# Kernel tuning notes

Hardware: AMD Instinct MI355X
Metric: run time of the kernel (lower is better)

## Reference

```python
import jax, jax.numpy as jnp
import numpy as np

N, E, F = 50000, 800000, 256
EPS = 1e-5


def _agg(h, src, dst, n):
    # gather src node features and sum into dst nodes (DGL copy_src + sum reduce)
    return jax.ops.segment_sum(h[src], dst, num_segments=n)


def _gcn_layer(h, src, dst, W, b):
    n = h.shape[0]
    h = _agg(h, src, dst, n)
    h = _agg(h, src, dst, n)  # update_all is called twice per layer
    return h @ W.T + b


def _batchnorm(h, gamma, beta):
    mean = jnp.mean(h, axis=0)
    var = jnp.mean(jnp.square(h - mean), axis=0)  # biased var, training mode
    return (h - mean) * jax.lax.rsqrt(var + EPS) * gamma + beta


def _branch(feature, src, dst, W1, b1, W2, b2, W3, b3, gamma, beta):
    h = _gcn_layer(feature, src, dst, W1, b1)
    h = _batchnorm(h, gamma, beta)
    h = _gcn_layer(h, src, dst, W2, b2)
    h = _gcn_layer(h, src, dst, W3, b3)
    return h


def setup_inputs() -> dict:
    key = jax.random.key(0)
    ks = jax.random.split(key, 12)
    s = 1.0 / np.sqrt(F)
    return {
        "feature": jax.random.normal(ks[0], (N, F), dtype=jnp.float32),
        "src1": jax.random.randint(ks[1], (E,), 0, N, dtype=jnp.int32),
        "dst1": jax.random.randint(ks[2], (E,), 0, N, dtype=jnp.int32),
        "src2": jax.random.randint(ks[3], (E,), 0, N, dtype=jnp.int32),
        "dst2": jax.random.randint(ks[4], (E,), 0, N, dtype=jnp.int32),
        "W1": jax.random.uniform(ks[5], (F, F), jnp.float32, -s, s),
        "b1": jax.random.uniform(ks[6], (F,), jnp.float32, -s, s),
        "W2": jax.random.uniform(ks[7], (F, F), jnp.float32, -s, s),
        "b2": jax.random.uniform(ks[8], (F,), jnp.float32, -s, s),
        "W3": jax.random.uniform(ks[9], (F, F), jnp.float32, -s, s),
        "b3": jax.random.uniform(ks[10], (F,), jnp.float32, -s, s),
        "gamma": jnp.ones((F,), jnp.float32),
        "beta": jnp.zeros((F,), jnp.float32),
    }


def reference(feature, src1, dst1, src2, dst2, W1, b1, W2, b2, W3, b3, gamma, beta):
    h1 = _branch(feature, src1, dst1, W1, b1, W2, b2, W3, b3, gamma, beta)
    h2 = _branch(feature, src2, dst2, W1, b1, W2, b2, W3, b3, gamma, beta)
    return h1.T @ h2  # [F, F]
```

## Files before the change

kernel.cpp:

```cpp
#include <hip/hip_runtime.h>
#include <hip/hip_fp16.h>

#define FDIM 256
#define GRAM_KS 96
#define NB 64


typedef _Float16 f16x8 __attribute__((ext_vector_type(8)));
typedef float f32x4 __attribute__((ext_vector_type(4)));

union H8 { uint2 u2[2]; f16x8 v; };

__device__ __forceinline__ f16x8 ldfrag(const __half* ldsT, int m, int g) {
  H8 h;
  h.u2[0] = *(const uint2*)(ldsT + m * 36 + g * 4);
  h.u2[1] = *(const uint2*)(ldsT + m * 36 + 16 + g * 4);
  return h.v;
}

__device__ __forceinline__ void h8acc(uint4 u, float* a) {
  float2 t;
  t = __half22float2(*(__half2*)&u.x); a[0] += t.x; a[1] += t.y;
  t = __half22float2(*(__half2*)&u.y); a[2] += t.x; a[3] += t.y;
  t = __half22float2(*(__half2*)&u.z); a[4] += t.x; a[5] += t.y;
  t = __half22float2(*(__half2*)&u.w); a[6] += t.x; a[7] += t.y;
}

__global__ void k_hist(const int* __restrict__ dst, int* __restrict__ deg, int E) {
  int e = blockIdx.x * 256 + threadIdx.x;
  if (e < E) atomicAdd(&deg[dst[e]], 1);
}

__global__ __launch_bounds__(256) void k_blksum(const int* __restrict__ deg,
    int* __restrict__ blksum, int n) {
  int b = blockIdx.x, tid = threadIdx.x;
  int base = b * 1024 + tid * 4;
  int s = 0;
#pragma unroll
  for (int k = 0; k < 4; ++k) if (base + k < n) s += deg[base + k];
  for (int off = 32; off; off >>= 1) s += __shfl_down(s, off);
  __shared__ int ws4[4];
  if ((tid & 63) == 0) ws4[tid >> 6] = s;
  __syncthreads();
  if (tid == 0) blksum[b] = ws4[0] + ws4[1] + ws4[2] + ws4[3];
}

__global__ void k_blkscan(const int* __restrict__ blksum, int* __restrict__ blkoff, int nblk) {
  int lane = threadIdx.x;
  int carry = 0;
  for (int base = 0; base < nblk; base += 64) {
    int v = (base + lane < nblk) ? blksum[base + lane] : 0;
    int x = v;
    for (int off = 1; off < 64; off <<= 1) { int y = __shfl_up(x, off); if (lane >= off) x += y; }
    if (base + lane < nblk) blkoff[base + lane] = carry + x - v;
    carry += __shfl(x, 63);
  }
}

__global__ __launch_bounds__(256) void k_scan_blk(const int* __restrict__ deg,
    const int* __restrict__ blkoff, int* __restrict__ rowptr, int* __restrict__ cursor, int n) {
  int b = blockIdx.x, tid = threadIdx.x;
  int base = b * 1024 + tid * 4;
  int v[4];
#pragma unroll
  for (int k = 0; k < 4; ++k) v[k] = (base + k < n) ? deg[base + k] : 0;
  int s = v[0] + v[1] + v[2] + v[3];
  int lane = tid & 63, w = tid >> 6;
  int x = s;
  for (int off = 1; off < 64; off <<= 1) { int y = __shfl_up(x, off); if (lane >= off) x += y; }
  __shared__ int wsum[4];
  if (lane == 63) wsum[w] = x;
  __syncthreads();
  int wadd = 0;
  for (int i = 0; i < w; ++i) wadd += wsum[i];
  int run = blkoff[b] + wadd + x - s;
#pragma unroll
  for (int k = 0; k < 4; ++k) {
    if (base + k < n) { rowptr[base + k] = run; cursor[base + k] = run; }
    run += v[k];
  }
  if (n >= base && n <= base + 4) rowptr[n] = run;
}

__global__ void k_binit(const int* __restrict__ rowptr, int* __restrict__ gcur,
    int N, int bshift) {
  int b = threadIdx.x;
  if (b < NB) {
    int idx = b << bshift;
    if (idx > N) idx = N;
    gcur[b] = rowptr[idx];
  }
}

__global__ __launch_bounds__(256) void k_part(const int* __restrict__ src,
    const int* __restrict__ dst, int* __restrict__ gcur, int2* __restrict__ pairs,
    int E, int bshift) {
  __shared__ int cnt[NB];
  __shared__ int lbase[NB];
  __shared__ int gbase[NB];
  __shared__ int tot;
  __shared__ int2 stg[4096];
  int tid = threadIdx.x;
  int e0 = blockIdx.x * 4096;
  if (tid < NB) cnt[tid] = 0;
  __syncthreads();
  int es[16], ed[16], lp[16];
#pragma unroll
  for (int k = 0; k < 16; ++k) {
    int e = e0 + k * 256 + tid;
    lp[k] = -1;
    if (e < E) {
      es[k] = src[e]; ed[k] = dst[e];
      lp[k] = atomicAdd(&cnt[ed[k] >> bshift], 1);
    }
  }
  __syncthreads();
  if (tid < NB) {
    int v = cnt[tid];
    int x = v;
    for (int off = 1; off < NB; off <<= 1) { int y = __shfl_up(x, off); if (tid >= off) x += y; }
    lbase[tid] = x - v;
    gbase[tid] = atomicAdd(&gcur[tid], v);
    if (tid == NB - 1) tot = x;
  }
  __syncthreads();
#pragma unroll
  for (int k = 0; k < 16; ++k) {
    if (lp[k] >= 0) stg[lbase[ed[k] >> bshift] + lp[k]] = make_int2(es[k], ed[k]);
  }
  __syncthreads();
  int T = tot;
  for (int i = tid; i < T; i += 256) {
    int2 p = stg[i];
    int b = p.y >> bshift;
    pairs[gbase[b] + (i - lbase[b])] = p;
  }
}

__global__ __launch_bounds__(512) void k_scat2(const int2* __restrict__ pairs,
    const int* __restrict__ rowptr, int* __restrict__ cursor, int* __restrict__ esrc,
    int N, int bshift) {
  int b = blockIdx.x;
  int i0 = b << bshift, i1 = (b + 1) << bshift;
  if (i0 > N) i0 = N;
  if (i1 > N) i1 = N;
  int lo = rowptr[i0], hi = rowptr[i1];
  for (int i = lo + threadIdx.x; i < hi; i += 512) {
    int2 p = pairs[i];
    int pos = atomicAdd(&cursor[p.y], 1);
    esrc[pos] = p.x;
  }
}

__global__ __launch_bounds__(256) void k_tr2(const float* __restrict__ W2,
    const float* __restrict__ W3, float* __restrict__ W2T, float* __restrict__ W3T) {
  __shared__ float tile[64][65];
  const float* src = blockIdx.z ? W3 : W2;
  float* dst = blockIdx.z ? W3T : W2T;
  int i0 = blockIdx.x * 64, j0 = blockIdx.y * 64;
  int tx = threadIdx.x & 63, ty = threadIdx.x >> 6;
#pragma unroll
  for (int m = 0; m < 16; ++m) {
    int r = ty * 16 + m;
    tile[r][tx] = src[(size_t)(i0 + r) * 256 + j0 + tx];
  }
  __syncthreads();
#pragma unroll
  for (int m = 0; m < 16; ++m) {
    int r = ty * 16 + m;
    dst[(size_t)(j0 + r) * 256 + i0 + tx] = tile[tx][r];
  }
}

__global__ __launch_bounds__(256) void k_f2h(const float* __restrict__ F,
    __half* __restrict__ H, int n4) {
  int i = blockIdx.x * 256 + threadIdx.x;
  if (i >= n4) return;
  float4 v = ((const float4*)F)[i];
  __half2 a = __floats2half2_rn(v.x, v.y);
  __half2 b = __floats2half2_rn(v.z, v.w);
  uint2 u; u.x = *(unsigned int*)&a; u.y = *(unsigned int*)&b;
  ((uint2*)H)[i] = u;
}

__global__ __launch_bounds__(256) void k_aggh(const __half* __restrict__ h,
    const int* __restrict__ rowptr, const int* __restrict__ esrc,
    __half* __restrict__ out, int n) {
  int wid = ((blockIdx.x * 256) + threadIdx.x) >> 6;
  int lane = threadIdx.x & 63;
  if (wid >= n) return;
  int half = lane >> 5, l5 = lane & 31;
  int beg = rowptr[wid], end = rowptr[wid + 1];
  const uint4* hv = (const uint4*)h;
  float a0[8] = {}, a1[8] = {}, a2[8] = {}, a3[8] = {};
  int e = beg + half;
  for (; e + 14 < end; e += 16) {
    int s0 = esrc[e], s1 = esrc[e + 2], s2 = esrc[e + 4], s3 = esrc[e + 6];
    int s4 = esrc[e + 8], s5 = esrc[e + 10], s6 = esrc[e + 12], s7 = esrc[e + 14];
    uint4 u0 = hv[(size_t)s0 * 32 + l5];
    uint4 u1 = hv[(size_t)s1 * 32 + l5];
    uint4 u2 = hv[(size_t)s2 * 32 + l5];
    uint4 u3 = hv[(size_t)s3 * 32 + l5];
    uint4 u4 = hv[(size_t)s4 * 32 + l5];
    uint4 u5 = hv[(size_t)s5 * 32 + l5];
    uint4 u6 = hv[(size_t)s6 * 32 + l5];
    uint4 u7 = hv[(size_t)s7 * 32 + l5];
    h8acc(u0, a0); h8acc(u1, a1); h8acc(u2, a2); h8acc(u3, a3);
    h8acc(u4, a0); h8acc(u5, a1); h8acc(u6, a2); h8acc(u7, a3);
  }
  for (; e + 6 < end; e += 8) {
    int s0 = esrc[e], s1 = esrc[e + 2], s2 = esrc[e + 4], s3 = esrc[e + 6];
    uint4 u0 = hv[(size_t)s0 * 32 + l5];
    uint4 u1 = hv[(size_t)s1 * 32 + l5];
    uint4 u2 = hv[(size_t)s2 * 32 + l5];
    uint4 u3 = hv[(size_t)s3 * 32 + l5];
    h8acc(u0, a0); h8acc(u1, a1); h8acc(u2, a2); h8acc(u3, a3);
  }
  for (; e < end; e += 2) {
    uint4 u = hv[(size_t)esrc[e] * 32 + l5];
    h8acc(u, a0);
  }
  float s[8];
#pragma unroll
  for (int j = 0; j < 8; ++j) {
    s[j] = (a0[j] + a1[j]) + (a2[j] + a3[j]);
    s[j] += __shfl_xor(s[j], 32);
    s[j] *= 0.25f;
  }
  if (half == 0) {
    __half2 h0 = __floats2half2_rn(s[0], s[1]);
    __half2 h1 = __floats2half2_rn(s[2], s[3]);
    __half2 h2 = __floats2half2_rn(s[4], s[5]);
    __half2 h3 = __floats2half2_rn(s[6], s[7]);
    uint4 uo;
    uo.x = *(unsigned int*)&h0; uo.y = *(unsigned int*)&h1;
    uo.z = *(unsigned int*)&h2; uo.w = *(unsigned int*)&h3;
    ((uint4*)out)[(size_t)wid * 32 + l5] = uo;
  }
}

__global__ __launch_bounds__(256) void k_aggv2(const float* __restrict__ in1,
    const float* __restrict__ in2,
    const int* __restrict__ rp1, const int* __restrict__ es1,
    const int* __restrict__ rp2, const int* __restrict__ es2,
    float* __restrict__ out1, float* __restrict__ out2, int n, int useDeg) {
  int t = blockIdx.x * 256 + threadIdx.x;
  int g = t >> 4;
  int sl = t & 15;
  if (g >= 2 * n) return;
  int which = (g >= n) ? 1 : 0;
  int node = which ? g - n : g;
  const int* rp = which ? rp2 : rp1;
  const int* es = which ? es2 : es1;
  const float* in = which ? in2 : in1;
  float* out = which ? out2 : out1;
  int beg = rp[node], end = rp[node + 1];
  float s = 0.f;
  if (useDeg) {
    for (int e = beg + sl; e < end; e += 16) {
      int v = es[e];
      s += (float)(rp[v + 1] - rp[v]);
    }
  } else {
    for (int e = beg + sl; e < end; e += 16) s += in[es[e]];
  }
#pragma unroll
  for (int off = 8; off; off >>= 1) s += __shfl_down(s, off, 16);
  if (sl == 0) out[node] = s;
}

__global__ __launch_bounds__(256) void k_gram_sym(const __half* __restrict__ Xm,
    float* __restrict__ partial, int N, float* __restrict__ mc) {
  __shared__ __half ldsA[128 * 36];
  __shared__ __half ldsB[128 * 36];
  int tid = threadIdx.x;
  int t = blockIdx.x;
  int i0 = (t == 2) ? 128 : 0;
  int j0 = (t == 0) ? 0 : 128;
  bool diag = (t != 1);
  int z = blockIdx.z;
  int chunk = (N + GRAM_KS - 1) / GRAM_KS;
  int rb = z * chunk, re = min(N, rb + chunk);
  int lane = tid & 63, w = tid >> 6;
  int g = lane >> 4;
  int lm = lane & 15;
  int wm = w >> 1, wn = w & 1;
  int sp = tid >> 4;
  int sc = (tid & 15) * 8;
  int cc = tid & 127, hh = tid >> 7;
  float xP = 0.f;
  f32x4 acc[4][4] = {};
  const __half* Bsrc = diag ? ldsA : ldsB;
  for (int rr = rb; rr < re; rr += 32) {
    int r0 = rr + 2 * sp, r1 = r0 + 1;
    uint4 a0 = {0,0,0,0}, a1 = {0,0,0,0}, b0 = {0,0,0,0}, b1 = {0,0,0,0};
    if (r0 < re) a0 = *(const uint4*)(Xm + (size_t)r0 * 256 + i0 + sc);
    if (r1 < re) a1 = *(const uint4*)(Xm + (size_t)r1 * 256 + i0 + sc);
    if (!diag) {
      if (r0 < re) b0 = *(const uint4*)(Xm + (size_t)r0 * 256 + j0 + sc);
      if (r1 < re) b1 = *(const uint4*)(Xm + (size_t)r1 * 256 + j0 + sc);
    }
    __syncthreads();
    {
      const unsigned short* pa0 = (const unsigned short*)&a0;
      const unsigned short* pa1 = (const unsigned short*)&a1;
      const unsigned short* pb0 = (const unsigned short*)&b0;
      const unsigned short* pb1 = (const unsigned short*)&b1;
#pragma unroll
      for (int j = 0; j < 8; ++j) {
        *(unsigned int*)(ldsA + (sc + j) * 36 + 2 * sp) =
            (unsigned int)pa0[j] | ((unsigned int)pa1[j] << 16);
        if (!diag)
          *(unsigned int*)(ldsB + (sc + j) * 36 + 2 * sp) =
              (unsigned int)pb0[j] | ((unsigned int)pb1[j] << 16);
      }
    }
    __syncthreads();
    if (diag && mc) {
      const __half* p = ldsA + cc * 36 + hh * 16;
#pragma unroll
      for (int k = 0; k < 16; ++k) xP += __half2float(p[k]);
    }
    f16x8 af[4];
#pragma unroll
    for (int fm = 0; fm < 4; ++fm) af[fm] = ldfrag(ldsA, wm * 64 + fm * 16 + lm, g);
#pragma unroll
    for (int fn = 0; fn < 4; ++fn) {
      f16x8 bf = ldfrag(Bsrc, wn * 64 + fn * 16 + lm, g);
#pragma unroll
      for (int fm = 0; fm < 4; ++fm)
        acc[fm][fn] = __builtin_amdgcn_mfma_f32_16x16x32_f16(af[fm], bf, acc[fm][fn], 0, 0, 0);
    }
  }
  float* pout = partial + (size_t)z * 65536;
#pragma unroll
  for (int fm = 0; fm < 4; ++fm) {
#pragma unroll
    for (int reg = 0; reg < 4; ++reg) {
      int row = i0 + wm * 64 + fm * 16 + g * 4 + reg;
#pragma unroll
      for (int fn = 0; fn < 4; ++fn) {
        int col = j0 + wn * 64 + fn * 16 + lm;
        pout[(size_t)row * 256 + col] = acc[fm][fn][reg];
      }
    }
  }
  if (diag && mc) {
    __syncthreads();
    float* fs = (float*)ldsA;
    fs[hh * 128 + cc] = xP;
    __syncthreads();
    if (tid < 128) atomicAdd(&mc[i0 + tid], (fs[tid] + fs[128 + tid]) * 16.0f);
  }
}

__global__ void k_gram_reduce_sym(const float* __restrict__ partial, float* __restrict__ C) {
  int idx = blockIdx.x * 256 + threadIdx.x;
  int i = idx >> 8, j = idx & 255;
  int sidx = (i >= 128 && j < 128) ? (j * 256 + i) : idx;
  float s = 0.f;
  for (int z = 0; z < GRAM_KS; ++z) s += partial[(size_t)z * 65536 + sidx];
  C[idx] = s * 256.0f;
}

__global__ __launch_bounds__(256) void k_gram(const __half* __restrict__ Xm,
    const __half* __restrict__ Ym, float* __restrict__ partial, int N,
    const float* __restrict__ wxA, const float* __restrict__ wxB, float* __restrict__ outX,
    const float* __restrict__ wyA, const float* __restrict__ wyB, float* __restrict__ outY) {
  __shared__ __half ldsA[128 * 36];
  __shared__ __half ldsB[128 * 36];
  __shared__ float wls[4][32];
  int tid = threadIdx.x;
  int i0 = blockIdx.x * 128, j0 = blockIdx.y * 128;
  int z = blockIdx.z;
  int chunk = (N + GRAM_KS - 1) / GRAM_KS;
  int rb = z * chunk, re = min(N, rb + chunk);
  int lane = tid & 63, w = tid >> 6;
  int g = lane >> 4;
  int lm = lane & 15;
  int wm = w >> 1, wn = w & 1;
  int sp = tid >> 4;
  int sc = (tid & 15) * 8;
  bool doX = (outX != nullptr) && (blockIdx.y == 0);
  bool doY = (outY != nullptr) && (blockIdx.x == 0);
  int cc = tid & 127, hh = tid >> 7;
  float xA = 0, xB = 0, xP = 0, yA = 0, yB = 0, yP = 0;
  f32x4 acc[4][4] = {};
  for (int rr = rb; rr < re; rr += 32) {
    int r0 = rr + 2 * sp, r1 = r0 + 1;
    uint4 a0 = {0,0,0,0}, a1 = {0,0,0,0}, b0 = {0,0,0,0}, b1 = {0,0,0,0};
    if (r0 < re) {
      a0 = *(const uint4*)(Xm + (size_t)r0 * 256 + i0 + sc);
      b0 = *(const uint4*)(Ym + (size_t)r0 * 256 + j0 + sc);
    }
    if (r1 < re) {
      a1 = *(const uint4*)(Xm + (size_t)r1 * 256 + i0 + sc);
      b1 = *(const uint4*)(Ym + (size_t)r1 * 256 + j0 + sc);
    }
    __syncthreads();
    {
      const unsigned short* pa0 = (const unsigned short*)&a0;
      const unsigned short* pa1 = (const unsigned short*)&a1;
      const unsigned short* pb0 = (const unsigned short*)&b0;
      const unsigned short* pb1 = (const unsigned short*)&b1;
#pragma unroll
      for (int j = 0; j < 8; ++j) {
        *(unsigned int*)(ldsA + (sc + j) * 36 + 2 * sp) =
            (unsigned int)pa0[j] | ((unsigned int)pa1[j] << 16);
        *(unsigned int*)(ldsB + (sc + j) * 36 + 2 * sp) =
            (unsigned int)pb0[j] | ((unsigned int)pb1[j] << 16);
      }
    }
    if (tid < 128) {
      int grp = tid >> 5, kk = tid & 31, rw = rr + kk;
      const float* wp = (grp == 0) ? wxA : (grp == 1) ? wxB : (grp == 2) ? wyA : wyB;
      wls[grp][kk] = (wp && rw < re) ? wp[rw] : 0.f;
    }
    __syncthreads();
    if (doX) {
      const __half* p = ldsA + cc * 36 + hh * 16;
#pragma unroll
      for (int k = 0; k < 16; ++k) {
        float v = __half2float(p[k]);
        xP += v; xA += v * wls[0][hh * 16 + k]; xB += v * wls[1][hh * 16 + k];
      }
    }
    if (doY) {
      const __half* p = ldsB + cc * 36 + hh * 16;
#pragma unroll
      for (int k = 0; k < 16; ++k) {
        float v = __half2float(p[k]);
        yP += v; yA += v * wls[2][hh * 16 + k]; yB += v * wls[3][hh * 16 + k];
      }
    }
    f16x8 af[4];
#pragma unroll
    for (int fm = 0; fm < 4; ++fm) af[fm] = ldfrag(ldsA, wm * 64 + fm * 16 + lm, g);
#pragma unroll
    for (int fn = 0; fn < 4; ++fn) {
      f16x8 bf = ldfrag(ldsB, wn * 64 + fn * 16 + lm, g);
#pragma unroll
      for (int fm = 0; fm < 4; ++fm)
        acc[fm][fn] = __builtin_amdgcn_mfma_f32_16x16x32_f16(af[fm], bf, acc[fm][fn], 0, 0, 0);
    }
  }
  float* pout = partial + (size_t)z * 65536;
#pragma unroll
  for (int fm = 0; fm < 4; ++fm) {
#pragma unroll
    for (int reg = 0; reg < 4; ++reg) {
      int row = i0 + wm * 64 + fm * 16 + g * 4 + reg;
#pragma unroll
      for (int fn = 0; fn < 4; ++fn) {
        int col = j0 + wn * 64 + fn * 16 + lm;
        pout[(size_t)row * 256 + col] = acc[fm][fn][reg];
      }
    }
  }
  const float S6 = 4096.0f;
  float* fs = (float*)ldsA;
  if (doX) {
    __syncthreads();
    fs[hh * 128 + cc] = xA;
    __syncthreads();
    if (tid < 128) atomicAdd(&outX[i0 + tid], (fs[tid] + fs[128 + tid]) * S6);
    __syncthreads();
    fs[hh * 128 + cc] = xB;
    __syncthreads();
    if (tid < 128) atomicAdd(&outX[256 + i0 + tid], (fs[tid] + fs[128 + tid]) * S6);
    __syncthreads();
    fs[hh * 128 + cc] = xP;
    __syncthreads();
    if (tid < 128) atomicAdd(&outX[512 + i0 + tid], (fs[tid] + fs[128 + tid]) * S6);
  }
  if (doY) {
    __syncthreads();
    fs[hh * 128 + cc] = yA;
    __syncthreads();
    if (tid < 128) atomicAdd(&outY[j0 + tid], (fs[tid] + fs[128 + tid]) * S6);
    __syncthreads();
    fs[hh * 128 + cc] = yB;
    __syncthreads();
    if (tid < 128) atomicAdd(&outY[256 + j0 + tid], (fs[tid] + fs[128 + tid]) * S6);
    __syncthreads();
    fs[hh * 128 + cc] = yP;
    __syncthreads();
    if (tid < 128) atomicAdd(&outY[512 + j0 + tid], (fs[tid] + fs[128 + tid]) * S6);
  }
}

__global__ void k_gram_reduce(const float* __restrict__ partial, float* __restrict__ C) {
  int idx = blockIdx.x * 256 + threadIdx.x;
  float s = 0.f;
  for (int z = 0; z < GRAM_KS; ++z) s += partial[(size_t)z * 65536 + idx];
  C[idx] = s * 16777216.0f;
}

__global__ __launch_bounds__(256) void k_dots(const float* __restrict__ d1,
    const float* __restrict__ e1, const float* __restrict__ d2,
    const float* __restrict__ e2, float* scal, int n) {
  float s[8] = {};
  for (int i = blockIdx.x * 256 + threadIdx.x; i < n; i += gridDim.x * 256) {
    float a = d1[i], b = e1[i], c = d2[i], d = e2[i];
    s[0] += b * d; s[1] += b * c; s[2] += b; s[3] += a * d;
    s[4] += a * c; s[5] += a; s[6] += d; s[7] += c;
  }
  __shared__ float red[4][8];
  int lane = threadIdx.x & 63, w = threadIdx.x >> 6;
#pragma unroll
  for (int j = 0; j < 8; ++j)
    for (int off = 32; off; off >>= 1) s[j] += __shfl_down(s[j], off);
  if (lane == 0)
#pragma unroll
    for (int j = 0; j < 8; ++j) red[w][j] = s[j];
  __syncthreads();
  if (threadIdx.x < 8) {
    int j = threadIdx.x;
    atomicAdd(&scal[j], red[0][j] + red[1][j] + red[2][j] + red[3][j]);
  }
}

__global__ __launch_bounds__(256) void k_quad(const float* __restrict__ C,
    const float* __restrict__ W1, const float* __restrict__ m_raw,
    float* __restrict__ t, float* __restrict__ mv) {
  __shared__ float w[256];
  __shared__ float r1[256], r2[256];
  int j = blockIdx.x, tid = threadIdx.x;
  w[tid] = W1[j * 256 + tid];
  __syncthreads();
  float v = 0.f;
  for (int k = 0; k < 256; ++k) v += w[k] * C[k * 256 + tid];
  r1[tid] = v * w[tid];
  r2[tid] = w[tid] * m_raw[tid];
  __syncthreads();
  for (int off = 128; off; off >>= 1) {
    if (tid < off) { r1[tid] += r1[tid + off]; r2[tid] += r2[tid + off]; }
    __syncthreads();
  }
  if (tid == 0) { t[j] = r1[0]; mv[j] = r2[0]; }
}

__global__ __launch_bounds__(256) void k_bncoef(const float* __restrict__ t,
    const float* __restrict__ mv, const float* __restrict__ b1,
    const float* __restrict__ gamma, const float* __restrict__ beta,
    const float* __restrict__ W2T, const float* __restrict__ W3T,
    const float* __restrict__ b2, float* Dv, float* xv, float* yv, int n) {
  __shared__ float c[256], u[256];
  int j = threadIdx.x;
  float invn = 1.f / (float)n;
  float mean = mv[j] * invn + b1[j];
  float E2 = t[j] * invn + 2.f * b1[j] * mv[j] * invn + b1[j] * b1[j];
  float var = E2 - mean * mean;
  float D = gamma[j] * rsqrtf(var + 1e-5f);
  Dv[j] = D;
  c[j] = D * (b1[j] - mean) + beta[j];
  __syncthreads();
  float uu = 0.f;
  for (int k = 0; k < 256; ++k) uu += W2T[k * 256 + j] * c[k];
  u[j] = uu;
  __syncthreads();
  float xx = 0.f, yy = 0.f;
  for (int k = 0; k < 256; ++k) {
    xx += W3T[k * 256 + j] * u[k];
    yy += W3T[k * 256 + j] * b2[k];
  }
  xv[j] = xx;
  yv[j] = yy;
}

__global__ __launch_bounds__(256) void k_mm_small(float* __restrict__ Cm,
    const float* __restrict__ A, const float* __restrict__ B,
    const float* __restrict__ s, int transA) {
  __shared__ float a[256];
  int i = blockIdx.x, j = threadIdx.x;
  float av = transA ? A[j * 256 + i] : A[i * 256 + j];
  a[j] = s ? av * s[j] : av;
  __syncthreads();
  float acc = 0.f;
  for (int k = 0; k < 256; ++k) acc += a[k] * B[k * 256 + j];
  Cm[i * 256 + j] = acc;
}

__global__ __launch_bounds__(256) void k_mv6(const float* __restrict__ R1,
    const float* __restrict__ R2, const float* __restrict__ pX,
    const float* __restrict__ qY, float* __restrict__ vout) {
  __shared__ float w[256];
  int b = blockIdx.x, j = threadIdx.x;
  const float* M = (b < 3) ? R1 : R2;
  const float* wv = (b < 3) ? (pX + b * 256) : (qY + (b - 3) * 256);
  w[j] = wv[j];
  __syncthreads();
  float s = 0.f;
  for (int k = 0; k < 256; ++k) s += M[k * 256 + j] * w[k];
  vout[b * 256 + j] = s;
}

__global__ __launch_bounds__(256) void k_mm_final(float* __restrict__ out,
    const float* __restrict__ R1, const float* __restrict__ T1,
    const float* __restrict__ vout,
    const float* __restrict__ x1, const float* __restrict__ x2,
    const float* __restrict__ yv, const float* __restrict__ b3,
    const float* __restrict__ scal, float fN) {
  __shared__ float a[256];
  int i = blockIdx.x, j = threadIdx.x;
  a[j] = R1[j * 256 + i];
  __syncthreads();
  float acc = 0.f;
  for (int k = 0; k < 256; ++k) acc += a[k] * T1[k * 256 + j];
  float s1 = scal[0] * x2[j] + scal[1] * yv[j] + scal[2] * b3[j];
  float s2 = scal[3] * x2[j] + scal[4] * yv[j] + scal[5] * b3[j];
  float s3 = scal[6] * x2[j] + scal[7] * yv[j] + fN * b3[j];
  acc += vout[i] * x2[j] + vout[256 + i] * yv[j] + vout[512 + i] * b3[j];
  acc += x1[i] * (vout[768 + j] + s1) + yv[i] * (vout[1024 + j] + s2)
       + b3[i] * (vout[1280 + j] + s3);
  out[i * 256 + j] = acc;
}

extern "C" void kernel_launch(void* const* d_in, const int* in_sizes, int n_in,
                              void* d_out, int out_size, void* d_ws, size_t ws_size,
                              hipStream_t stream) {
  const float* feature = (const float*)d_in[0];
  const int* src1 = (const int*)d_in[1];
  const int* dst1 = (const int*)d_in[2];
  const int* src2 = (const int*)d_in[3];
  const int* dst2 = (const int*)d_in[4];
  const float* W1 = (const float*)d_in[5];
  const float* b1 = (const float*)d_in[6];
  const float* W2 = (const float*)d_in[7];
  const float* b2 = (const float*)d_in[8];
  const float* W3 = (const float*)d_in[9];
  const float* b3 = (const float*)d_in[10];
  const float* gamma = (const float*)d_in[11];
  const float* beta = (const float*)d_in[12];
  const int N = in_sizes[0] / FDIM;
  const int E = in_sizes[1];
  float* out = (float*)d_out;

  size_t NF = (size_t)N * FDIM;
  __half* FH = (__half*)d_ws;
  __half* Xh = FH + NF;
  __half* Yh = Xh + NF;
  __half* G2A = Yh + NF;
  float* partial = (float*)(G2A + NF);
  int* rowptr1 = (int*)(partial + (size_t)GRAM_KS * 65536);
  int* rowptr2 = rowptr1 + (N + 1);
  int* cursor = rowptr2 + (N + 1);
  int* esrc1 = cursor + N;
  int* esrc2 = esrc1 + E;
  float* vtmp1 = (float*)(esrc2 + E);
  float* vtmp2 = vtmp1 + N;
  float* d1 = vtmp2 + N; float* e1 = d1 + N; float* d2 = e1 + N; float* e2 = d2 + N;
  float* C = e2 + N;
  float* mcA = C + 65536;
  float* mcB = mcA + 256;
  float* pX = mcB + 256;
  float* qY = pX + 768;
  float* scal = qY + 768;
  float* tq = scal + 16; float* mv = tq + 256;
  float* Dv = mv + 256; float* x1 = Dv + 256; float* x2 = x1 + 256; float* yv = x2 + 256;
  float* Q = yv + 256; float* R1 = Q + 65536; float* R2 = R1 + 65536;
  float* Z = R2 + 65536; float* T1 = Z + 65536;
  float* W2T = T1 + 65536; float* W3T = W2T + 65536;
  float* vout = W3T + 65536;
  int* blksum = (int*)(vout + 1536);
  int* blkoff = blksum + 1024;
  int* gcur = blkoff + 1024;
  int2* pairs = (int2*)partial;

  const int eb = (E + 255) / 256;
  const int aggb = (N + 3) / 4;
  const int avb2 = (2 * N * 16 + 255) / 256;
  const int nblk = (N + 1023) / 1024;
  int bshift = 0;
  while (((N - 1) >> bshift) >= NB) ++bshift;
  const int nbk = ((N - 1) >> bshift) + 1;
  const int pb = (E + 4095) / 4096;

  auto build = [&](const int* s_, const int* d_, int* rp, int* es) {
    hipMemsetAsync(cursor, 0, (size_t)N * sizeof(int), stream);
    k_hist<<<eb, 256, 0, stream>>>(d_, cursor, E);
    k_blksum<<<nblk, 256, 0, stream>>>(cursor, blksum, N);
    k_blkscan<<<1, 64, 0, stream>>>(blksum, blkoff, nblk);
    k_scan_blk<<<nblk, 256, 0, stream>>>(cursor, blkoff, rp, cursor, N);
    k_binit<<<1, 64, 0, stream>>>(rp, gcur, N, bshift);
    k_part<<<pb, 256, 0, stream>>>(s_, d_, gcur, pairs, E, bshift);
    k_scat2<<<nbk, 512, 0, stream>>>(pairs, rp, cursor, es, N, bshift);
  };

  k_tr2<<<dim3(4, 4, 2), 256, 0, stream>>>(W2, W3, W2T, W3T);
  k_f2h<<<(int)((NF / 4 + 255) / 256), 256, 0, stream>>>(feature, FH, (int)(NF / 4));
  build(src1, dst1, rowptr1, esrc1);
  build(src2, dst2, rowptr2, esrc2);
  hipMemsetAsync(mcA, 0, (256 * 2 + 768 * 2 + 16) * sizeof(float), stream);

  k_aggv2<<<avb2, 256, 0, stream>>>(nullptr, nullptr, rowptr1, esrc1, rowptr2, esrc2,
                                    d1, d2, N, 1);
  k_aggv2<<<avb2, 256, 0, stream>>>(d1, d2, rowptr1, esrc1, rowptr2, esrc2,
                                    vtmp1, vtmp2, N, 0);
  k_aggv2<<<avb2, 256, 0, stream>>>(vtmp1, vtmp2, rowptr1, esrc1, rowptr2, esrc2,
                                    e1, e2, N, 0);
  k_dots<<<64, 256, 0, stream>>>(d1, e1, d2, e2, scal, N);

  auto do_branch = [&](const int* rp, const int* es, __half* G2dst,
                       float* mc, float* xvec, float* Rdst) {
    k_aggh<<<aggb, 256, 0, stream>>>(FH, rp, es, Xh, N);
    k_aggh<<<aggb, 256, 0, stream>>>(Xh, rp, es, Yh, N);
    k_gram_sym<<<dim3(3, 1, GRAM_KS), 256, 0, stream>>>(Yh, partial, N, mc);
    k_gram_reduce_sym<<<256, 256, 0, stream>>>(partial, C);
    k_quad<<<256, 256, 0, stream>>>(C, W1, mc, tq, mv);
    k_bncoef<<<1, 256, 0, stream>>>(tq, mv, b1, gamma, beta, W2T, W3T, b2, Dv, xvec, yv, N);
    k_mm_small<<<256, 256, 0, stream>>>(Q, W1, W2T, Dv, 1);
    k_mm_small<<<256, 256, 0, stream>>>(Rdst, Q, W3T, nullptr, 0);
    k_aggh<<<aggb, 256, 0, stream>>>(Yh, rp, es, Xh, N);
    k_aggh<<<aggb, 256, 0, stream>>>(Xh, rp, es, Yh, N);
    k_aggh<<<aggb, 256, 0, stream>>>(Yh, rp, es, Xh, N);
    k_aggh<<<aggb, 256, 0, stream>>>(Xh, rp, es, G2dst, N);
  };

  do_branch(rowptr1, esrc1, G2A, mcA, x1, R1);
  do_branch(rowptr2, esrc2, Yh, mcB, x2, R2);

  k_gram<<<dim3(2, 2, GRAM_KS), 256, 0, stream>>>(G2A, Yh, partial, N,
      e2, d2, pX, e1, d1, qY);
  k_gram_reduce<<<256, 256, 0, stream>>>(partial, Z);

  k_mm_small<<<256, 256, 0, stream>>>(T1, Z, R2, nullptr, 0);
  k_mv6<<<6, 256, 0, stream>>>(R1, R2, pX, qY, vout);
  k_mm_final<<<256, 256, 0, stream>>>(out, R1, T1, vout, x1, x2, yv, b3, scal, (float)N);
}
```

Baseline: 1.365 ms.

## Store fp16 features in column-sliced layout and aggregate per 32-column slice

Half-precision node features move from row-major to eight column slices of 32 halves each, so each slice (about 3.2 MB) is more likely to stay in cache during gather. The aggregation kernel is rewritten so each block works on one slice and each wave handles a contiguous range of nodes, with 16 lanes per edge and four edges in flight. The gram kernels switch to the new addressing. In exchange, the edge index list is read once per slice (eight times in total) and each gathered access is only 64 bytes, which may cost memory efficiency.

```diff
diff --git a/kernel.cpp b/kernel.cpp
--- a/kernel.cpp
+++ b/kernel.cpp
@@ -10,20 +10,17 @@
 typedef float f32x4 __attribute__((ext_vector_type(4)));
 
 union H8 { uint2 u2[2]; f16x8 v; };
+
+__device__ __forceinline__ const uint4* sl4(const __half* X, int n, int r, int col) {
+  return (const uint4*)(X + (size_t)(col >> 5) * ((size_t)n * 32)
+                          + (size_t)r * 32 + (col & 31));
+}
 
 __device__ __forceinline__ f16x8 ldfrag(const __half* ldsT, int m, int g) {
   H8 h;
   h.u2[0] = *(const uint2*)(ldsT + m * 36 + g * 4);
   h.u2[1] = *(const uint2*)(ldsT + m * 36 + 16 + g * 4);
   return h.v;
-}
-
-__device__ __forceinline__ void h8acc(uint4 u, float* a) {
-  float2 t;
-  t = __half22float2(*(__half2*)&u.x); a[0] += t.x; a[1] += t.y;
-  t = __half22float2(*(__half2*)&u.y); a[2] += t.x; a[3] += t.y;
-  t = __half22float2(*(__half2*)&u.z); a[4] += t.x; a[5] += t.y;
-  t = __half22float2(*(__half2*)&u.w); a[6] += t.x; a[7] += t.y;
 }
 
 __global__ void k_hist(const int* __restrict__ dst, int* __restrict__ deg, int E) {
@@ -173,69 +170,78 @@
 }
 
 __global__ __launch_bounds__(256) void k_f2h(const float* __restrict__ F,
-    __half* __restrict__ H, int n4) {
-  int i = blockIdx.x * 256 + threadIdx.x;
-  if (i >= n4) return;
-  float4 v = ((const float4*)F)[i];
-  __half2 a = __floats2half2_rn(v.x, v.y);
-  __half2 b = __floats2half2_rn(v.z, v.w);
-  uint2 u; u.x = *(unsigned int*)&a; u.y = *(unsigned int*)&b;
-  ((uint2*)H)[i] = u;
-}
-
-__global__ __launch_bounds__(256) void k_aggh(const __half* __restrict__ h,
+    __half* __restrict__ H, int n) {
+  int t = blockIdx.x * 256 + threadIdx.x;
+  if (t >= n * 32) return;
+  int r = t >> 5, c8 = t & 31;
+  int col = c8 * 8;
+  const float4* f4 = (const float4*)(F + (size_t)r * 256 + col);
+  float4 v0 = f4[0], v1 = f4[1];
+  __half2 h0 = __floats2half2_rn(v0.x, v0.y);
+  __half2 h1 = __floats2half2_rn(v0.z, v0.w);
+  __half2 h2 = __floats2half2_rn(v1.x, v1.y);
+  __half2 h3 = __floats2half2_rn(v1.z, v1.w);
+  uint4 u;
+  u.x = *(unsigned int*)&h0; u.y = *(unsigned int*)&h1;
+  u.z = *(unsigned int*)&h2; u.w = *(unsigned int*)&h3;
+  *(uint4*)(H + (size_t)(col >> 5) * ((size_t)n * 32) + (size_t)r * 32 + (col & 31)) = u;
+}
+
+__global__ __launch_bounds__(256) void k_aggs(const __half* __restrict__ h,
     const int* __restrict__ rowptr, const int* __restrict__ esrc,
-    __half* __restrict__ out, int n) {
-  int wid = ((blockIdx.x * 256) + threadIdx.x) >> 6;
+    __half* __restrict__ out, int n, int nwchunk) {
+  int chunk = blockIdx.x & 7;
+  int wslot = (blockIdx.x >> 3) * 4 + (threadIdx.x >> 6);
   int lane = threadIdx.x & 63;
-  if (wid >= n) return;
-  int half = lane >> 5, l5 = lane & 31;
-  int beg = rowptr[wid], end = rowptr[wid + 1];
-  const uint4* hv = (const uint4*)h;
-  float a0[8] = {}, a1[8] = {}, a2[8] = {}, a3[8] = {};
-  int e = beg + half;
-  for (; e + 14 < end; e += 16) {
-    int s0 = esrc[e], s1 = esrc[e + 2], s2 = esrc[e + 4], s3 = esrc[e + 6];
-    int s4 = esrc[e + 8], s5 = esrc[e + 10], s6 = esrc[e + 12], s7 = esrc[e + 14];
-    uint4 u0 = hv[(size_t)s0 * 32 + l5];
-    uint4 u1 = hv[(size_t)s1 * 32 + l5];
-    uint4 u2 = hv[(size_t)s2 * 32 + l5];
-    uint4 u3 = hv[(size_t)s3 * 32 + l5];
-    uint4 u4 = hv[(size_t)s4 * 32 + l5];
-    uint4 u5 = hv[(size_t)s5 * 32 + l5];
-    uint4 u6 = hv[(size_t)s6 * 32 + l5];
-    uint4 u7 = hv[(size_t)s7 * 32 + l5];
-    h8acc(u0, a0); h8acc(u1, a1); h8acc(u2, a2); h8acc(u3, a3);
-    h8acc(u4, a0); h8acc(u5, a1); h8acc(u6, a2); h8acc(u7, a3);
-  }
-  for (; e + 6 < end; e += 8) {
-    int s0 = esrc[e], s1 = esrc[e + 2], s2 = esrc[e + 4], s3 = esrc[e + 6];
-    uint4 u0 = hv[(size_t)s0 * 32 + l5];
-    uint4 u1 = hv[(size_t)s1 * 32 + l5];
-    uint4 u2 = hv[(size_t)s2 * 32 + l5];
-    uint4 u3 = hv[(size_t)s3 * 32 + l5];
-    h8acc(u0, a0); h8acc(u1, a1); h8acc(u2, a2); h8acc(u3, a3);
-  }
-  for (; e < end; e += 2) {
-    uint4 u = hv[(size_t)esrc[e] * 32 + l5];
-    h8acc(u, a0);
-  }
-  float s[8];
-#pragma unroll
-  for (int j = 0; j < 8; ++j) {
-    s[j] = (a0[j] + a1[j]) + (a2[j] + a3[j]);
-    s[j] += __shfl_xor(s[j], 32);
-    s[j] *= 0.25f;
-  }
-  if (half == 0) {
-    __half2 h0 = __floats2half2_rn(s[0], s[1]);
-    __half2 h1 = __floats2half2_rn(s[2], s[3]);
-    __half2 h2 = __floats2half2_rn(s[4], s[5]);
-    __half2 h3 = __floats2half2_rn(s[6], s[7]);
-    uint4 uo;
-    uo.x = *(unsigned int*)&h0; uo.y = *(unsigned int*)&h1;
-    uo.z = *(unsigned int*)&h2; uo.w = *(unsigned int*)&h3;
-    ((uint4*)out)[(size_t)wid * 32 + l5] = uo;
+  int eslot = lane >> 4, l16 = lane & 15;
+  const __half* hs = h + (size_t)chunk * ((size_t)n * 32);
+  __half* os = out + (size_t)chunk * ((size_t)n * 32);
+  int npw = (n + nwchunk - 1) / nwchunk;
+  int w0 = wslot * npw, w1 = min(n, w0 + npw);
+  for (int wid = w0; wid < w1; ++wid) {
+    int beg = rowptr[wid], end = rowptr[wid + 1];
+    float p0 = 0, p1 = 0, q0 = 0, q1 = 0, r0 = 0, r1 = 0, s0f = 0, s1f = 0;
+    int e = beg + eslot;
+    for (; e + 12 < end; e += 16) {
+      int s0 = __builtin_nontemporal_load(esrc + e);
+      int s1 = __builtin_nontemporal_load(esrc + e + 4);
+      int s2 = __builtin_nontemporal_load(esrc + e + 8);
+      int s3 = __builtin_nontemporal_load(esrc + e + 12);
+      unsigned u0 = *(const unsigned*)(hs + (size_t)s0 * 32 + l16 * 2);
+      unsigned u1 = *(const unsigned*)(hs + (size_t)s1 * 32 + l16 * 2);
+      unsigned u2 = *(const unsigned*)(hs + (size_t)s2 * 32 + l16 * 2);
+      unsigned u3 = *(const unsigned*)(hs + (size_t)s3 * 32 + l16 * 2);
+      float2 f0 = __half22float2(*(__half2*)&u0);
+      float2 f1 = __half22float2(*(__half2*)&u1);
+      float2 f2 = __half22float2(*(__half2*)&u2);
+      float2 f3 = __half22float2(*(__half2*)&u3);
+      p0 += f0.x; p1 += f0.y; q0 += f1.x; q1 += f1.y;
+      r0 += f2.x; r1 += f2.y; s0f += f3.x; s1f += f3.y;
+    }
+    for (; e + 4 < end; e += 8) {
+      int s0 = __builtin_nontemporal_load(esrc + e);
+      int s1 = __builtin_nontemporal_load(esrc + e + 4);
+      unsigned u0 = *(const unsigned*)(hs + (size_t)s0 * 32 + l16 * 2);
+      unsigned u1 = *(const unsigned*)(hs + (size_t)s1 * 32 + l16 * 2);
+      float2 f0 = __half22float2(*(__half2*)&u0);
+      float2 f1 = __half22float2(*(__half2*)&u1);
+      p0 += f0.x; p1 += f0.y; q0 += f1.x; q1 += f1.y;
+    }
+    for (; e < end; e += 4) {
+      int s0 = __builtin_nontemporal_load(esrc + e);
+      unsigned u0 = *(const unsigned*)(hs + (size_t)s0 * 32 + l16 * 2);
+      float2 f0 = __half22float2(*(__half2*)&u0);
+      p0 += f0.x; p1 += f0.y;
+    }
+    float a0 = (p0 + q0) + (r0 + s0f);
+    float a1 = (p1 + q1) + (r1 + s1f);
+    a0 += __shfl_xor(a0, 16); a1 += __shfl_xor(a1, 16);
+    a0 += __shfl_xor(a0, 32); a1 += __shfl_xor(a1, 32);
+    if (eslot == 0) {
+      __half2 hv = __floats2half2_rn(a0 * 0.25f, a1 * 0.25f);
+      __builtin_nontemporal_store(*(unsigned int*)&hv,
+          (unsigned int*)(os + (size_t)wid * 32 + l16 * 2));
+    }
   }
 }
 
@@ -294,11 +300,11 @@
   for (int rr = rb; rr < re; rr += 32) {
     int r0 = rr + 2 * sp, r1 = r0 + 1;
     uint4 a0 = {0,0,0,0}, a1 = {0,0,0,0}, b0 = {0,0,0,0}, b1 = {0,0,0,0};
-    if (r0 < re) a0 = *(const uint4*)(Xm + (size_t)r0 * 256 + i0 + sc);
-    if (r1 < re) a1 = *(const uint4*)(Xm + (size_t)r1 * 256 + i0 + sc);
+    if (r0 < re) a0 = *sl4(Xm, N, r0, i0 + sc);
+    if (r1 < re) a1 = *sl4(Xm, N, r1, i0 + sc);
     if (!diag) {
-      if (r0 < re) b0 = *(const uint4*)(Xm + (size_t)r0 * 256 + j0 + sc);
-      if (r1 < re) b1 = *(const uint4*)(Xm + (size_t)r1 * 256 + j0 + sc);
+      if (r0 < re) b0 = *sl4(Xm, N, r0, j0 + sc);
+      if (r1 < re) b1 = *sl4(Xm, N, r1, j0 + sc);
     }
     __syncthreads();
     {
@@ -390,12 +396,12 @@
     int r0 = rr + 2 * sp, r1 = r0 + 1;
     uint4 a0 = {0,0,0,0}, a1 = {0,0,0,0}, b0 = {0,0,0,0}, b1 = {0,0,0,0};
     if (r0 < re) {
-      a0 = *(const uint4*)(Xm + (size_t)r0 * 256 + i0 + sc);
-      b0 = *(const uint4*)(Ym + (size_t)r0 * 256 + j0 + sc);
+      a0 = *sl4(Xm, N, r0, i0 + sc);
+      b0 = *sl4(Ym, N, r0, j0 + sc);
     }
     if (r1 < re) {
-      a1 = *(const uint4*)(Xm + (size_t)r1 * 256 + i0 + sc);
-      b1 = *(const uint4*)(Ym + (size_t)r1 * 256 + j0 + sc);
+      a1 = *sl4(Xm, N, r1, i0 + sc);
+      b1 = *sl4(Ym, N, r1, j0 + sc);
     }
     __syncthreads();
     {
@@ -668,13 +674,14 @@
   int2* pairs = (int2*)partial;
 
   const int eb = (E + 255) / 256;
-  const int aggb = (N + 3) / 4;
   const int avb2 = (2 * N * 16 + 255) / 256;
   const int nblk = (N + 1023) / 1024;
   int bshift = 0;
   while (((N - 1) >> bshift) >= NB) ++bshift;
   const int nbk = ((N - 1) >> bshift) + 1;
   const int pb = (E + 4095) / 4096;
+  const int aggblocks = 8192;
+  const int nwchunk = (aggblocks / 8) * 4;
 
   auto build = [&](const int* s_, const int* d_, int* rp, int* es) {
     hipMemsetAsync(cursor, 0, (size_t)N * sizeof(int), stream);
@@ -688,7 +695,7 @@
   };
 
   k_tr2<<<dim3(4, 4, 2), 256, 0, stream>>>(W2, W3, W2T, W3T);
-  k_f2h<<<(int)((NF / 4 + 255) / 256), 256, 0, stream>>>(feature, FH, (int)(NF / 4));
+  k_f2h<<<(N * 32 + 255) / 256, 256, 0, stream>>>(feature, FH, N);
   build(src1, dst1, rowptr1, esrc1);
   build(src2, dst2, rowptr2, esrc2);
   hipMemsetAsync(mcA, 0, (256 * 2 + 768 * 2 + 16) * sizeof(float), stream);
@@ -703,18 +710,18 @@
 
   auto do_branch = [&](const int* rp, const int* es, __half* G2dst,
                        float* mc, float* xvec, float* Rdst) {
-    k_aggh<<<aggb, 256, 0, stream>>>(FH, rp, es, Xh, N);
-    k_aggh<<<aggb, 256, 0, stream>>>(Xh, rp, es, Yh, N);
+    k_aggs<<<aggblocks, 256, 0, stream>>>(FH, rp, es, Xh, N, nwchunk);
+    k_aggs<<<aggblocks, 256, 0, stream>>>(Xh, rp, es, Yh, N, nwchunk);
     k_gram_sym<<<dim3(3, 1, GRAM_KS), 256, 0, stream>>>(Yh, partial, N, mc);
     k_gram_reduce_sym<<<256, 256, 0, stream>>>(partial, C);
     k_quad<<<256, 256, 0, stream>>>(C, W1, mc, tq, mv);
     k_bncoef<<<1, 256, 0, stream>>>(tq, mv, b1, gamma, beta, W2T, W3T, b2, Dv, xvec, yv, N);
     k_mm_small<<<256, 256, 0, stream>>>(Q, W1, W2T, Dv, 1);
     k_mm_small<<<256, 256, 0, stream>>>(Rdst, Q, W3T, nullptr, 0);
-    k_aggh<<<aggb, 256, 0, stream>>>(Yh, rp, es, Xh, N);
-    k_aggh<<<aggb, 256, 0, stream>>>(Xh, rp, es, Yh, N);
-    k_aggh<<<aggb, 256, 0, stream>>>(Yh, rp, es, Xh, N);
-    k_aggh<<<aggb, 256, 0, stream>>>(Xh, rp, es, G2dst, N);
+    k_aggs<<<aggblocks, 256, 0, stream>>>(Yh, rp, es, Xh, N, nwchunk);
+    k_aggs<<<aggblocks, 256, 0, stream>>>(Xh, rp, es, Yh, N, nwchunk);
+    k_aggs<<<aggblocks, 256, 0, stream>>>(Yh, rp, es, Xh, N, nwchunk);
+    k_aggs<<<aggblocks, 256, 0, stream>>>(Xh, rp, es, G2dst, N, nwchunk);
   };
 
   do_branch(rowptr1, esrc1, G2A, mcA, x1, R1);
```

Measured after the change: 2.412 ms. +76.7%, slower.
